# Kernel tuning notes

Measured on AMD Instinct MI355X. Metric: run time of the kernel, lower is better.

Reference implementation:

```python
import jax, jax.numpy as jnp
import numpy as np

B, L, H, N, DM = 16, 32768, 64, 16, 32


def setup_inputs() -> dict:
    key = jax.random.key(0)
    ks = jax.random.split(key, 16)
    inp = {}
    inp['x'] = jax.random.normal(ks[0], (B, L, H), dtype=jnp.float32)
    inp['control_parameters'] = jax.random.uniform(ks[1], (B, 2), dtype=jnp.float32)
    inp['W0'] = jax.random.normal(ks[2], (2, DM), dtype=jnp.float32) / np.sqrt(2.0)
    inp['b0'] = jnp.zeros((DM,), dtype=jnp.float32)
    inp['W1'] = jax.random.normal(ks[3], (DM, DM), dtype=jnp.float32) / np.sqrt(DM)
    inp['b1'] = jnp.zeros((DM,), dtype=jnp.float32)
    inp['W2'] = jax.random.normal(ks[4], (DM, DM), dtype=jnp.float32) / np.sqrt(DM)
    inp['b2'] = jnp.zeros((DM,), dtype=jnp.float32)
    # BlockV1 input linear
    inp['W_lin'] = jax.random.normal(ks[5], (H, H), dtype=jnp.float32) / np.sqrt(H)
    inp['b_lin'] = jnp.zeros((H,), dtype=jnp.float32)
    # DSSM / S4D parameters (S4D-Lin init)
    log_dt_min, log_dt_max = np.log(1e-3), np.log(1e-1)
    inp['log_dt'] = (log_dt_min + (log_dt_max - log_dt_min)
                     * jax.random.uniform(ks[6], (H,), dtype=jnp.float32))
    inp['A_re'] = -0.5 * jnp.ones((H, N), dtype=jnp.float32)
    inp['A_im'] = jnp.broadcast_to(np.pi * jnp.arange(N, dtype=jnp.float32), (H, N)).copy()
    inp['C_re'] = jax.random.normal(ks[7], (H, N), dtype=jnp.float32) / np.sqrt(2.0)
    inp['C_im'] = jax.random.normal(ks[8], (H, N), dtype=jnp.float32) / np.sqrt(2.0)
    inp['D'] = jax.random.normal(ks[9], (H,), dtype=jnp.float32)
    # FiLM: Linear(DM, 2*H) -> (gamma, beta)
    inp['W_film'] = jax.random.normal(ks[10], (DM, 2 * H), dtype=jnp.float32) / np.sqrt(DM)
    inp['b_film'] = jnp.zeros((2 * H,), dtype=jnp.float32)
    return inp


def _s4d_kernel(log_dt, A_re, A_im, C_re, C_im, length):
    # Diagonal SSM (S4D) convolution kernel via ZOH discretization.
    dt = jnp.exp(log_dt)[:, None]                      # [H,1]
    A = A_re + 1j * A_im                               # [H,N]
    dtA = dt * A                                       # [H,N]
    C = (C_re + 1j * C_im) * (jnp.exp(dtA) - 1.0) / A  # [H,N]
    t = jnp.arange(length, dtype=jnp.float32)          # [L]
    # Vandermonde: K[h,l] = 2 * Re( sum_n C[h,n] * exp(dtA[h,n])^l )
    vand = jnp.exp(dtA[:, :, None] * t)                # [H,N,L] complex
    return 2.0 * jnp.einsum('hn,hnl->hl', C, vand).real


def reference(x, control_parameters, W0, b0, W1, b1, W2, b2,
              W_lin, b_lin, log_dt, A_re, A_im, C_re, C_im, D,
              W_film, b_film):
    gelu = jax.nn.gelu
    # control-parameter MLP -> conditioning vector [B, DM]
    cond = gelu(control_parameters @ W0 + b0)
    cond = gelu(cond @ W1 + b1)
    cond = gelu(cond @ W2 + b2)
    # BlockV1: Linear + act
    h = gelu(x @ W_lin + b_lin)          # [B,L,H]
    u = jnp.swapaxes(h, 1, 2)            # [B,H,L]
    length = u.shape[-1]
    # S4D global convolution via FFT (linear, non-circular)
    K = _s4d_kernel(log_dt, A_re, A_im, C_re, C_im, length)   # [H,L]
    n = 2 * length
    Kf = jnp.fft.rfft(K, n=n)            # [H, n//2+1]
    uf = jnp.fft.rfft(u, n=n)            # [B,H, n//2+1]
    y = jnp.fft.irfft(uf * Kf, n=n)[..., :length] + D[:, None] * u  # [B,H,L]
    y = jnp.swapaxes(y, 1, 2)            # [B,L,H]
    # FiLM conditioning (no batch norm)
    gb = cond @ W_film + b_film          # [B, 2H]
    g, b = jnp.split(gb, 2, axis=-1)     # [B,H] each
    y = gelu(y * g[:, None, :] + b[:, None, :])
    # side-chain gate: elementwise multiply with input
    return x * y
```

## Files before the change

### kernel.cpp

```cpp
#include <hip/hip_runtime.h>
#include <hip/hip_bf16.h>
#include <math.h>

#define B_ 16
#define L_ 32768
#define H_ 64
#define N_ 16
#define DM_ 32
#define TS_ 16
#define US_ 68
#define NG_ 8

typedef __attribute__((ext_vector_type(8))) short short8;
typedef __attribute__((ext_vector_type(4))) float floatx4;
typedef __attribute__((ext_vector_type(2))) float f32x2;

__device__ __forceinline__ float fast_gelu(float v) {
    float z = fmaf(0.044715f * v, v * v, v) * 0.7978845608028654f;
#if __has_builtin(__builtin_amdgcn_exp2f) && __has_builtin(__builtin_amdgcn_rcpf)
    float e = __builtin_amdgcn_exp2f(z * 2.8853900817779268f);
    float t = 1.0f - 2.0f * __builtin_amdgcn_rcpf(e + 1.0f);
#else
    float t = tanhf(z);
#endif
    return 0.5f * v * (1.0f + t);
}

__device__ __forceinline__ unsigned short bf16_rne(float f) {
    unsigned u = __float_as_uint(f);
    return (unsigned short)((u + 0x7FFFu + ((u >> 16) & 1u)) >> 16);
}
__device__ __forceinline__ float bf16_tof(unsigned short h) {
    return __uint_as_float(((unsigned)h) << 16);
}
__device__ __forceinline__ void cvt8(const float* f, short8* hi, short8* lo) {
    union { unsigned u[4]; short8 s; } Hh, Ll;
    #pragma unroll
    for (int jp = 0; jp < 4; ++jp) {
        unsigned short h0 = bf16_rne(f[2*jp]), h1 = bf16_rne(f[2*jp+1]);
        Hh.u[jp] = (unsigned)h0 | ((unsigned)h1 << 16);
        float l0 = f[2*jp]   - bf16_tof(h0);
        float l1 = f[2*jp+1] - bf16_tof(h1);
        Ll.u[jp] = (unsigned)bf16_rne(l0) | ((unsigned)bf16_rne(l1) << 16);
    }
    *hi = Hh.s; *lo = Ll.s;
}

__device__ __forceinline__ void pk_step(f32x2& s, f32x2 w, f32x2 uv0) {
    f32x2 t;
    asm("v_pk_fma_f32 %0, %1, %2, %3 op_sel:[1,1,0] op_sel_hi:[1,0,1] neg_lo:[1,0,0]"
        : "=v"(t) : "v"(w), "v"(s), "v"(uv0));
    asm("v_pk_fma_f32 %0, %1, %0, %2 op_sel_hi:[0,1,1]"
        : "+v"(s) : "v"(w), "v"(t));
}
__device__ __forceinline__ void pk_acc(f32x2& y, f32x2 c, f32x2 s) {
    asm("v_pk_fma_f32 %0, %1, %2, %0"
        : "+v"(y) : "v"(c), "v"(s));
}

__global__ void cond_film_kernel(const float* __restrict__ cp,
    const float* __restrict__ W0, const float* __restrict__ b0,
    const float* __restrict__ W1, const float* __restrict__ b1,
    const float* __restrict__ W2, const float* __restrict__ b2,
    const float* __restrict__ Wf, const float* __restrict__ bf,
    float* __restrict__ film) {
    __shared__ float ca[B_][DM_];
    __shared__ float cb[B_][DM_];
    int tid = threadIdx.x;
    int b = tid >> 5, j = tid & 31;
    float acc = fmaf(cp[b*2+0], W0[j], fmaf(cp[b*2+1], W0[DM_+j], b0[j]));
    ca[b][j] = fast_gelu(acc);
    __syncthreads();
    acc = b1[j];
    #pragma unroll
    for (int i = 0; i < DM_; ++i) acc = fmaf(ca[b][i], W1[i*DM_+j], acc);
    cb[b][j] = fast_gelu(acc);
    __syncthreads();
    acc = b2[j];
    #pragma unroll
    for (int i = 0; i < DM_; ++i) acc = fmaf(cb[b][i], W2[i*DM_+j], acc);
    float c2 = fast_gelu(acc);
    __syncthreads();
    ca[b][j] = c2;
    __syncthreads();
    #pragma unroll
    for (int t = 0; t < 4; ++t) {
        int k = j + DM_*t;
        float a = bf[k];
        #pragma unroll
        for (int i = 0; i < DM_; ++i) a = fmaf(ca[b][i], Wf[i*2*H_+k], a);
        film[b*2*H_ + k] = a;
    }
}

__global__ void coef_kernel(const float* __restrict__ log_dt,
    const float* __restrict__ A_re, const float* __restrict__ A_im,
    const float* __restrict__ C_re, const float* __restrict__ C_im,
    float* __restrict__ coef, float Tf) {
    int g = blockIdx.x * blockDim.x + threadIdx.x;
    if (g >= H_*N_) return;
    int h = g >> 4, n = g & 15;
    float dt = expf(log_dt[h]);
    float Ar = A_re[h*N_+n], Ai = A_im[h*N_+n];
    float ar = dt*Ar, ai = dt*Ai;
    float er = expf(ar);
    float wr = er * cosf(ai), wi = er * sinf(ai);
    float eT = expf(Tf * ar);
    float aT = Tf * ai;
    float wTr = eT * cosf(aT), wTi = eT * sinf(aT);
    float d  = Ar*Ar + Ai*Ai;
    float nr = wr - 1.0f, ni = wi;
    float qr = (nr*Ar + ni*Ai) / d;
    float qi = (ni*Ar - nr*Ai) / d;
    float Cr = C_re[h*N_+n], Ci = C_im[h*N_+n];
    float cr = 2.0f * (Cr*qr - Ci*qi);
    float ci = 2.0f * (Cr*qi + Ci*qr);
    coef[(n*6+0)*H_+h] = wr;
    coef[(n*6+1)*H_+h] = wi;
    coef[(n*6+2)*H_+h] = wTr;
    coef[(n*6+3)*H_+h] = wTi;
    coef[(n*6+4)*H_+h] = cr;
    coef[(n*6+5)*H_+h] = ci;
}


__global__ void scan_agg_kernel(const float* __restrict__ states,
                                const float* __restrict__ coef,
                                float* __restrict__ agg, int Cc, int G) {
    int t = blockIdx.x * blockDim.x + threadIdx.x;
    int h = t & 63, n = (t >> 6) & 15, g = (t >> 10) & (NG_-1), b = t >> 13;
    float wTr = coef[(n*6+2)*H_+h], wTi = coef[(n*6+3)*H_+h];
    const float2* sp = (const float2*)states
        + ((size_t)(b*Cc + g*G))*N_*H_ + (size_t)n*H_ + h;
    const int stride = N_*H_;
    float car = 0.f, cai = 0.f;
    float2 buf[8];
    #pragma unroll
    for (int i = 0; i < 8; ++i) buf[i] = sp[(size_t)i*stride];
    for (int cg = 0; cg < G; cg += 8) {
        float2 nb[8];
        #pragma unroll
        for (int i = 0; i < 8; ++i)
            nb[i] = (cg + 8 + i < G) ? sp[(size_t)(cg+8+i)*stride]
                                     : make_float2(0.f, 0.f);
        #pragma unroll
        for (int i = 0; i < 8; ++i) {
            float2 v = buf[i];
            float nr2 = fmaf(wTr, car, fmaf(-wTi, cai, v.x));
            float ni2 = fmaf(wTr, cai, fmaf( wTi, car, v.y));
            car = nr2; cai = ni2;
            buf[i] = nb[i];
        }
    }
    ((float2*)agg)[t] = make_float2(car, cai);
}

__global__ void scan_group_kernel(float* __restrict__ agg,
                                  const float* __restrict__ coef, int lg2G) {
    int t = blockIdx.x * blockDim.x + threadIdx.x;
    int h = t & 63, n = (t >> 6) & 15, b = t >> 10;
    float wr = coef[(n*6+2)*H_+h], wi = coef[(n*6+3)*H_+h];
    for (int i = 0; i < lg2G; ++i) {
        float nr = wr*wr - wi*wi, ni = 2.f*wr*wi;
        wr = nr; wi = ni;
    }
    float car = 0.f, cai = 0.f;
    float2* ap = (float2*)agg + (size_t)b*NG_*1024 + (size_t)n*64 + h;
    #pragma unroll
    for (int g = 0; g < NG_; ++g) {
        float2 v = ap[(size_t)g*1024];
        ap[(size_t)g*1024] = make_float2(car, cai);
        float nr = fmaf(wr, car, fmaf(-wi, cai, v.x));
        float ni = fmaf(wr, cai, fmaf( wi, car, v.y));
        car = nr; cai = ni;
    }
}

__global__ void scan_fix_kernel(float* __restrict__ states,
                                const float* __restrict__ coef,
                                const float* __restrict__ agg, int Cc, int G) {
    int t = blockIdx.x * blockDim.x + threadIdx.x;
    int h = t & 63, n = (t >> 6) & 15, g = (t >> 10) & (NG_-1), b = t >> 13;
    float wTr = coef[(n*6+2)*H_+h], wTi = coef[(n*6+3)*H_+h];
    float2* sp = (float2*)states
        + ((size_t)(b*Cc + g*G))*N_*H_ + (size_t)n*H_ + h;
    const int stride = N_*H_;
    float2 c0 = ((const float2*)agg)[t];
    float car = c0.x, cai = c0.y;
    float2 buf[8];
    #pragma unroll
    for (int i = 0; i < 8; ++i) buf[i] = sp[(size_t)i*stride];
    for (int cg = 0; cg < G; cg += 8) {
        float2 nb[8];
        #pragma unroll
        for (int i = 0; i < 8; ++i)
            nb[i] = (cg + 8 + i < G) ? sp[(size_t)(cg+8+i)*stride]
                                     : make_float2(0.f, 0.f);
        #pragma unroll
        for (int i = 0; i < 8; ++i) {
            float2 v = buf[i];
            sp[(size_t)(cg+i)*stride] = make_float2(car, cai);
            float nr2 = fmaf(wTr, car, fmaf(-wTi, cai, v.x));
            float ni2 = fmaf(wTr, cai, fmaf( wTi, car, v.y));
            car = nr2; cai = ni2;
            buf[i] = nb[i];
        }
    }
}

template<int PHASE, int CC>
__global__ __launch_bounds__(256, 3)
void gemm_scan_kernel(const float* __restrict__ x,
                      const float* __restrict__ W_lin, const float* __restrict__ b_lin,
                      const float* __restrict__ coef, float* __restrict__ states,
                      const float* __restrict__ D, const float* __restrict__ film,
                      float* __restrict__ out) {
    constexpr int TT = L_/CC;
    __shared__ __align__(16) unsigned short Wf[16*64*8];
    __shared__ float uld[4][TS_*US_];
    __shared__ float xld[(PHASE==3) ? 4*TS_*US_ : 4];
    const int lane = threadIdx.x & 63;
    const int wv   = threadIdx.x >> 6;
    const int q    = blockIdx.x*4 + wv;
    const int b    = q / CC;
    const int c    = q % CC;
    const int m    = lane & 15;
    const int quad = lane >> 4;

    for (int kt = 0; kt < 2; ++kt)
        for (int nt = 0; nt < 4; ++nt) {
            float f[8];
            #pragma unroll
            for (int j = 0; j < 8; ++j)
                f[j] = W_lin[(kt*32 + quad*8 + j)*H_ + nt*16 + m];
            short8 hi, lo;
            cvt8(f, &hi, &lo);
            ((short8*)Wf)[(kt*4 + nt)*64 + lane]     = hi;
            ((short8*)Wf)[((2+kt)*4 + nt)*64 + lane] = lo;
        }

    f32x2 w2[N_], s2[N_], c2[N_];
    float g_ = 0.f, be_ = 0.f, Dh = 0.f;
    #pragma unroll
    for (int n = 0; n < N_; ++n) {
        w2[n].x = coef[(n*6+0)*H_ + lane];
        w2[n].y = coef[(n*6+1)*H_ + lane];
    }
    if (PHASE == 1) {
        #pragma unroll
        for (int n = 0; n < N_; ++n) s2[n] = (f32x2){0.f, 0.f};
    } else {
        #pragma unroll
        for (int n = 0; n < N_; ++n) {
            c2[n].x = coef[(n*6+4)*H_ + lane];
            c2[n].y = coef[(n*6+5)*H_ + lane];
            size_t idx = (((size_t)q*N_ + n)*H_ + lane)*2;
            s2[n] = *(const f32x2*)(states + idx);
        }
        g_  = film[b*2*H_ + lane];
        be_ = film[b*2*H_ + H_ + lane];
        Dh  = D[lane];
    }
    float blv[4];
    #pragma unroll
    for (int nt = 0; nt < 4; ++nt) blv[nt] = b_lin[nt*16 + m];

    const float* xp = x + ((size_t)b*L_ + (size_t)c*TT)*H_;
    float* op = out + ((size_t)b*L_ + (size_t)c*TT)*H_;
    float* myu = uld[wv];
    float* myx = (PHASE==3) ? &xld[wv*TS_*US_] : nullptr;

    for (int s = 0; s < TT/TS_; ++s) {
        const float* xs = xp + s*TS_*H_;
        short8 ah[2], al[2];
        #pragma unroll
        for (int kt = 0; kt < 2; ++kt) {
            const float* src = xs + m*H_ + kt*32 + quad*8;
            float4 v0 = *(const float4*)(src);
            float4 v1 = *(const float4*)(src + 4);
            if (PHASE == 3) {
                float* dst = &myx[m*US_ + kt*32 + quad*8];
                *(float4*)(dst)     = v0;
                *(float4*)(dst + 4) = v1;
            }
            float f[8] = {v0.x, v0.y, v0.z, v0.w, v1.x, v1.y, v1.z, v1.w};
            cvt8(f, &ah[kt], &al[kt]);
        }
        #pragma unroll
        for (int nt = 0; nt < 4; ++nt) {
            floatx4 acc = {0.f, 0.f, 0.f, 0.f};
            #pragma unroll
            for (int kt = 0; kt < 2; ++kt) {
                short8 bh = ((short8*)Wf)[(kt*4 + nt)*64 + lane];
                short8 bl = ((short8*)Wf)[((2+kt)*4 + nt)*64 + lane];
                acc = __builtin_amdgcn_mfma_f32_16x16x32_bf16(ah[kt], bh, acc, 0, 0, 0);
                acc = __builtin_amdgcn_mfma_f32_16x16x32_bf16(al[kt], bh, acc, 0, 0, 0);
                acc = __builtin_amdgcn_mfma_f32_16x16x32_bf16(ah[kt], bl, acc, 0, 0, 0);
            }
            #pragma unroll
            for (int r = 0; r < 4; ++r) {
                int row = quad*4 + r;
                float uv = fast_gelu(acc[r] + blv[nt]);
                myu[row*US_ + nt*16 + m] = uv;
            }
        }
        float uvc = myu[lane];
        float xgc = (PHASE==3) ? myx[lane] : 0.f;
        for (int l = 0; l < TS_; ++l) {
            int ln = (l+1) & (TS_-1);
            float uvn = myu[ln*US_ + lane];
            float xgn = (PHASE==3) ? myx[ln*US_ + lane] : 0.f;
            f32x2 uv0 = {uvc, 0.f};
            if (PHASE == 1) {
                #pragma unroll
                for (int n = 0; n < N_; ++n) pk_step(s2[n], w2[n], uv0);
            } else {
                f32x2 y2 = {0.f, 0.f};
                #pragma unroll
                for (int n = 0; n < N_; ++n) {
                    pk_step(s2[n], w2[n], uv0);
                    pk_acc(y2, c2[n], s2[n]);
                }
                float y  = fmaf(Dh, uvc, y2.x - y2.y);
                float yg = fast_gelu(fmaf(y, g_, be_));
                op[(s*TS_ + l)*H_ + lane] = xgc * yg;
            }
            uvc = uvn; xgc = xgn;
        }
    }
    if (PHASE == 1) {
        #pragma unroll
        for (int n = 0; n < N_; ++n) {
            size_t idx = (((size_t)q*N_ + n)*H_ + lane)*2;
            *(f32x2*)(states + idx) = s2[n];
        }
    }
}

extern "C" void kernel_launch(void* const* d_in, const int* in_sizes, int n_in,
                              void* d_out, int out_size, void* d_ws, size_t ws_size,
                              hipStream_t stream) {
    const float* x     = (const float*)d_in[0];
    const float* cp    = (const float*)d_in[1];
    const float* W0    = (const float*)d_in[2];
    const float* b0    = (const float*)d_in[3];
    const float* W1    = (const float*)d_in[4];
    const float* b1    = (const float*)d_in[5];
    const float* W2    = (const float*)d_in[6];
    const float* b2    = (const float*)d_in[7];
    const float* W_lin = (const float*)d_in[8];
    const float* b_lin = (const float*)d_in[9];
    const float* log_dt= (const float*)d_in[10];
    const float* A_re  = (const float*)d_in[11];
    const float* A_im  = (const float*)d_in[12];
    const float* C_re  = (const float*)d_in[13];
    const float* C_im  = (const float*)d_in[14];
    const float* D     = (const float*)d_in[15];
    const float* W_f   = (const float*)d_in[16];
    const float* b_f   = (const float*)d_in[17];
    float* out = (float*)d_out;

    float* film   = (float*)d_ws;
    float* coef   = film + B_*2*H_;
    float* states = coef + 6*H_*N_;

    cond_film_kernel<<<1, 512, 0, stream>>>(cp, W0, b0, W1, b1, W2, b2,
                                            W_f, b_f, film);

    size_t need64 = (size_t)(B_*2*H_ + 6*H_*N_)*4
                  + (size_t)B_*512*N_*H_*2*4
                  + (size_t)B_*NG_*N_*H_*2*4;
    if (ws_size >= need64) {
        const int Cc = 512, G = 64, lg2G = 6;
        float* agg = states + (size_t)B_*Cc*N_*H_*2;
        coef_kernel<<<4, 256, 0, stream>>>(log_dt, A_re, A_im, C_re, C_im,
                                           coef, (float)(L_/Cc));
        gemm_scan_kernel<1,512><<<(B_*512)/4, 256, 0, stream>>>(
            x, W_lin, b_lin, coef, states, nullptr, nullptr, nullptr);
        scan_agg_kernel<<<(B_*NG_*N_*H_)/256, 256, 0, stream>>>(states, coef,
                                                                agg, Cc, G);
        scan_group_kernel<<<(B_*N_*H_)/256, 256, 0, stream>>>(agg, coef, lg2G);
        scan_fix_kernel<<<(B_*NG_*N_*H_)/256, 256, 0, stream>>>(states, coef,
                                                                agg, Cc, G);
        gemm_scan_kernel<3,512><<<(B_*512)/4, 256, 0, stream>>>(
            x, W_lin, b_lin, coef, states, D, film, out);
    } else {
        const int Cc = 256, G = 32, lg2G = 5;
        float* agg = states + (size_t)B_*Cc*N_*H_*2;
        coef_kernel<<<4, 256, 0, stream>>>(log_dt, A_re, A_im, C_re, C_im,
                                           coef, (float)(L_/Cc));
        gemm_scan_kernel<1,256><<<(B_*256)/4, 256, 0, stream>>>(
            x, W_lin, b_lin, coef, states, nullptr, nullptr, nullptr);
        scan_agg_kernel<<<(B_*NG_*N_*H_)/256, 256, 0, stream>>>(states, coef,
                                                                agg, Cc, G);
        scan_group_kernel<<<(B_*N_*H_)/256, 256, 0, stream>>>(agg, coef, lg2G);
        scan_fix_kernel<<<(B_*NG_*N_*H_)/256, 256, 0, stream>>>(states, coef,
                                                                agg, Cc, G);
        gemm_scan_kernel<3,256><<<(B_*256)/4, 256, 0, stream>>>(
            x, W_lin, b_lin, coef, states, D, film, out);
    }
}
```

Baseline: 495.4 us.

## Materialize GELU activations in phase one and use lightweight output scan kernel

The first scan pass now stores the GELU(linear) activations to a workspace buffer. A new scan_out kernel reads those activations and x to finish the second scan pass, so the MFMA GEMM and GELU are no longer recomputed. This trades recomputation for about 256MB of extra global memory traffic, and the path only runs when the workspace is large enough.

```diff
diff --git a/kernel.cpp b/kernel.cpp
--- a/kernel.cpp
+++ b/kernel.cpp
@@ -208,13 +208,13 @@
     }
 }
 
-template<int PHASE, int CC>
+template<int PHASE, int CC, bool UST>
 __global__ __launch_bounds__(256, 3)
 void gemm_scan_kernel(const float* __restrict__ x,
                       const float* __restrict__ W_lin, const float* __restrict__ b_lin,
                       const float* __restrict__ coef, float* __restrict__ states,
                       const float* __restrict__ D, const float* __restrict__ film,
-                      float* __restrict__ out) {
+                      float* __restrict__ out, float* __restrict__ ubuf) {
     constexpr int TT = L_/CC;
     __shared__ __align__(16) unsigned short Wf[16*64*8];
     __shared__ float uld[4][TS_*US_];
@@ -265,8 +265,10 @@
     #pragma unroll
     for (int nt = 0; nt < 4; ++nt) blv[nt] = b_lin[nt*16 + m];
 
-    const float* xp = x + ((size_t)b*L_ + (size_t)c*TT)*H_;
-    float* op = out + ((size_t)b*L_ + (size_t)c*TT)*H_;
+    const size_t base = ((size_t)b*L_ + (size_t)c*TT)*H_;
+    const float* xp = x + base;
+    float* op = out + base;
+    float* ubp = UST ? (ubuf + base) : nullptr;
     float* myu = uld[wv];
     float* myx = (PHASE==3) ? &xld[wv*TS_*US_] : nullptr;
 
@@ -312,6 +314,7 @@
             float xgn = (PHASE==3) ? myx[ln*US_ + lane] : 0.f;
             f32x2 uv0 = {uvc, 0.f};
             if (PHASE == 1) {
+                if (UST) ubp[(s*TS_ + l)*H_ + lane] = uvc;
                 #pragma unroll
                 for (int n = 0; n < N_; ++n) pk_step(s2[n], w2[n], uv0);
             } else {
@@ -333,6 +336,68 @@
         for (int n = 0; n < N_; ++n) {
             size_t idx = (((size_t)q*N_ + n)*H_ + lane)*2;
             *(f32x2*)(states + idx) = s2[n];
+        }
+    }
+}
+
+template<int CC>
+__global__ __launch_bounds__(256, 3)
+void scan_out_kernel(const float* __restrict__ u, const float* __restrict__ x,
+                     const float* __restrict__ coef, const float* __restrict__ states,
+                     const float* __restrict__ D, const float* __restrict__ film,
+                     float* __restrict__ out) {
+    constexpr int TT = L_/CC;
+    constexpr int BL = 8;
+    const int lane = threadIdx.x & 63;
+    const int wv   = threadIdx.x >> 6;
+    const int q    = blockIdx.x*4 + wv;
+    const int b    = q / CC;
+    f32x2 w2[N_], s2[N_], c2[N_];
+    #pragma unroll
+    for (int n = 0; n < N_; ++n) {
+        w2[n].x = coef[(n*6+0)*H_ + lane];
+        w2[n].y = coef[(n*6+1)*H_ + lane];
+        c2[n].x = coef[(n*6+4)*H_ + lane];
+        c2[n].y = coef[(n*6+5)*H_ + lane];
+        size_t idx = (((size_t)q*N_ + n)*H_ + lane)*2;
+        s2[n] = *(const f32x2*)(states + idx);
+    }
+    const float g_  = film[b*2*H_ + lane];
+    const float be_ = film[b*2*H_ + H_ + lane];
+    const float Dh  = D[lane];
+    const size_t base = ((size_t)b*L_ + (size_t)(q % CC)*TT)*H_;
+    const float* up = u + base;
+    const float* xp = x + base;
+    float* op = out + base;
+
+    float ub[BL], xb[BL];
+    #pragma unroll
+    for (int i = 0; i < BL; ++i) {
+        ub[i] = up[i*H_ + lane];
+        xb[i] = xp[i*H_ + lane];
+    }
+    for (int t0 = 0; t0 < TT; t0 += BL) {
+        float nu[BL] = {}, nx[BL] = {};
+        if (t0 + BL < TT) {
+            #pragma unroll
+            for (int i = 0; i < BL; ++i) {
+                nu[i] = up[(t0+BL+i)*H_ + lane];
+                nx[i] = xp[(t0+BL+i)*H_ + lane];
+            }
+        }
+        #pragma unroll
+        for (int i = 0; i < BL; ++i) {
+            f32x2 uv0 = {ub[i], 0.f};
+            f32x2 y2 = {0.f, 0.f};
+            #pragma unroll
+            for (int n = 0; n < N_; ++n) {
+                pk_step(s2[n], w2[n], uv0);
+                pk_acc(y2, c2[n], s2[n]);
+            }
+            float y  = fmaf(Dh, ub[i], y2.x - y2.y);
+            float yg = fast_gelu(fmaf(y, g_, be_));
+            op[(t0+i)*H_ + lane] = xb[i] * yg;
+            ub[i] = nu[i]; xb[i] = nx[i];
         }
     }
 }
@@ -367,36 +432,55 @@
     cond_film_kernel<<<1, 512, 0, stream>>>(cp, W0, b0, W1, b1, W2, b2,
                                             W_f, b_f, film);
 
-    size_t need64 = (size_t)(B_*2*H_ + 6*H_*N_)*4
-                  + (size_t)B_*512*N_*H_*2*4
-                  + (size_t)B_*NG_*N_*H_*2*4;
-    if (ws_size >= need64) {
+    const size_t head = (size_t)(B_*2*H_ + 6*H_*N_);
+    const size_t st512 = (size_t)B_*512*N_*H_*2;
+    const size_t aggsz = (size_t)B_*NG_*N_*H_*2;
+    const size_t usz   = (size_t)B_*L_*H_;
+    size_t need_u  = (head + st512 + aggsz + usz)*4;
+    size_t need64  = (head + st512 + aggsz)*4;
+
+    if (ws_size >= need_u) {
         const int Cc = 512, G = 64, lg2G = 6;
-        float* agg = states + (size_t)B_*Cc*N_*H_*2;
+        float* agg  = states + st512;
+        float* ubuf = agg + aggsz;
         coef_kernel<<<4, 256, 0, stream>>>(log_dt, A_re, A_im, C_re, C_im,
                                            coef, (float)(L_/Cc));
-        gemm_scan_kernel<1,512><<<(B_*512)/4, 256, 0, stream>>>(
-            x, W_lin, b_lin, coef, states, nullptr, nullptr, nullptr);
+        gemm_scan_kernel<1,512,true><<<(B_*512)/4, 256, 0, stream>>>(
+            x, W_lin, b_lin, coef, states, nullptr, nullptr, nullptr, ubuf);
         scan_agg_kernel<<<(B_*NG_*N_*H_)/256, 256, 0, stream>>>(states, coef,
                                                                 agg, Cc, G);
         scan_group_kernel<<<(B_*N_*H_)/256, 256, 0, stream>>>(agg, coef, lg2G);
         scan_fix_kernel<<<(B_*NG_*N_*H_)/256, 256, 0, stream>>>(states, coef,
                                                                 agg, Cc, G);
-        gemm_scan_kernel<3,512><<<(B_*512)/4, 256, 0, stream>>>(
-            x, W_lin, b_lin, coef, states, D, film, out);
+        scan_out_kernel<512><<<(B_*512)/4, 256, 0, stream>>>(
+            ubuf, x, coef, states, D, film, out);
+    } else if (ws_size >= need64) {
+        const int Cc = 512, G = 64, lg2G = 6;
+        float* agg = states + st512;
+        coef_kernel<<<4, 256, 0, stream>>>(log_dt, A_re, A_im, C_re, C_im,
+                                           coef, (float)(L_/Cc));
+        gemm_scan_kernel<1,512,false><<<(B_*512)/4, 256, 0, stream>>>(
+            x, W_lin, b_lin, coef, states, nullptr, nullptr, nullptr, nullptr);
+        scan_agg_kernel<<<(B_*NG_*N_*H_)/256, 256, 0, stream>>>(states, coef,
+                                                                agg, Cc, G);
+        scan_group_kernel<<<(B_*N_*H_)/256, 256, 0, stream>>>(agg, coef, lg2G);
+        scan_fix_kernel<<<(B_*NG_*N_*H_)/256, 256, 0, stream>>>(states, coef,
+                                                                agg, Cc, G);
+        gemm_scan_kernel<3,512,false><<<(B_*512)/4, 256, 0, stream>>>(
+            x, W_lin, b_lin, coef, states, D, film, out, nullptr);
     } else {
         const int Cc = 256, G = 32, lg2G = 5;
-        float* agg = states + (size_t)B_*Cc*N_*H_*2;
+        float* agg = states + (size_t)B_*256*N_*H_*2;
         coef_kernel<<<4, 256, 0, stream>>>(log_dt, A_re, A_im, C_re, C_im,
                                            coef, (float)(L_/Cc));
-        gemm_scan_kernel<1,256><<<(B_*256)/4, 256, 0, stream>>>(
-            x, W_lin, b_lin, coef, states, nullptr, nullptr, nullptr);
+        gemm_scan_kernel<1,256,false><<<(B_*256)/4, 256, 0, stream>>>(
+            x, W_lin, b_lin, coef, states, nullptr, nullptr, nullptr, nullptr);
         scan_agg_kernel<<<(B_*NG_*N_*H_)/256, 256, 0, stream>>>(states, coef,
                                                                 agg, Cc, G);
         scan_group_kernel<<<(B_*N_*H_)/256, 256, 0, stream>>>(agg, coef, lg2G);
         scan_fix_kernel<<<(B_*NG_*N_*H_)/256, 256, 0, stream>>>(states, coef,
                                                                 agg, Cc, G);
-        gemm_scan_kernel<3,256><<<(B_*256)/4, 256, 0, stream>>>(
-            x, W_lin, b_lin, coef, states, D, film, out);
-    }
-}
+        gemm_scan_kernel<3,256,false><<<(B_*256)/4, 256, 0, stream>>>(
+            x, W_lin, b_lin, coef, states, D, film, out, nullptr);
+    }
+}
```

After: 440.4 us. 11.1% less time.
